# Performance work log

Measured on AMD Instinct MI355X. Metric: run time of the kernel, lower is better.

Reference implementation:

```python
import jax, jax.numpy as jnp
import numpy as np

EPS = 1e-6
K = 20
NEG_SLOPE = 0.2

def knn_idx(x, k):
    # x: (B, D, N) flattened vector features; returns (B, N, k) neighbor indices
    inner = -2.0 * jnp.einsum('bdn,bdm->bnm', x, x)
    xx = jnp.sum(x * x, axis=1)  # (B, N)
    pd = -xx[:, :, None] - inner - xx[:, None, :]  # negative squared distance
    _, idx = jax.lax.top_k(pd, k)
    return idx

def get_graph_feature(x, k):
    # x: (B, C, 3, N) -> (B, 2C, 3, N, k) edge features (nbr - ctr, ctr)
    B, C, _, N = x.shape
    idx = knn_idx(x.reshape(B, C * 3, N), k)           # (B, N, k)
    feat = jnp.transpose(x, (0, 3, 1, 2))              # (B, N, C, 3)
    nb = jax.vmap(lambda f, i: f[i])(feat, idx)        # (B, N, k, C, 3)
    ctr = jnp.broadcast_to(feat[:, :, None], nb.shape)
    out = jnp.concatenate([nb - ctr, ctr], axis=3)     # (B, N, k, 2C, 3)
    return jnp.transpose(out, (0, 3, 4, 1, 2))

def vn_batchnorm(x, gamma, beta):
    # x: (B, C, 3, ...); BatchNorm (training stats) applied to vector norms
    norm = jnp.linalg.norm(x, axis=2) + EPS            # (B, C, ...)
    axes = (0,) + tuple(range(2, norm.ndim))
    mu = jnp.mean(norm, axis=axes, keepdims=True)
    var = jnp.var(norm, axis=axes, keepdims=True)
    shape = (1, -1) + (1,) * (norm.ndim - 2)
    nbn = (norm - mu) / jnp.sqrt(var + 1e-5) * gamma.reshape(shape) + beta.reshape(shape)
    return x / norm[:, :, None] * nbn[:, :, None]

def vn_linear_leakyrelu(x, w_feat, w_dir, gamma, beta):
    # x: (B, Cin, 3, ...) -> (B, Cout, 3, ...)
    p = jnp.einsum('oc,bc...->bo...', w_feat, x)
    p = vn_batchnorm(p, gamma, beta)
    d = jnp.einsum('oc,bc...->bo...', w_dir, x)
    dot = jnp.sum(p * d, axis=2, keepdims=True)
    dsq = jnp.sum(d * d, axis=2, keepdims=True)
    proj = p - (dot / (dsq + EPS)) * d
    return NEG_SLOPE * p + (1.0 - NEG_SLOPE) * jnp.where(dot >= 0, p, proj)

def _forward(x, w1, d1, g1, b1, w2, d2, g2, b2, w3, d3, g3, b3, w4, d4, g4, b4, w5, d5, g5, b5):
    h = jnp.transpose(x, (0, 2, 1))[:, None]           # (B, 1, 3, N)
    h = vn_linear_leakyrelu(get_graph_feature(h, K), w1, d1, g1, b1)
    x1 = jnp.mean(h, axis=-1)                          # mean_pool over k: (B, 21, 3, N)
    h = vn_linear_leakyrelu(get_graph_feature(x1, K), w2, d2, g2, b2)
    x2 = jnp.mean(h, axis=-1)                          # (B, 21, 3, N)
    h = vn_linear_leakyrelu(get_graph_feature(x2, K), w3, d3, g3, b3)
    x3 = jnp.mean(h, axis=-1)                          # (B, 42, 3, N)
    h = vn_linear_leakyrelu(get_graph_feature(x3, K), w4, d4, g4, b4)
    x4 = jnp.mean(h, axis=-1)                          # (B, 85, 3, N)
    cat = jnp.concatenate([x1, x2, x3, x4], axis=1)    # (B, 169, 3, N)
    return vn_linear_leakyrelu(cat, w5, d5, g5, b5)    # (B, 341, 3, N)

def setup_inputs():
    key = jax.random.key(0)
    B, N = 8, 1024
    d = {"x": jax.random.normal(key, (B, N, 3), dtype=jnp.float32)}
    feat_shapes = {"1": (21, 2), "2": (21, 42), "3": (42, 42), "4": (85, 84), "5": (341, 169)}
    dir_out = {"1": 21, "2": 21, "3": 42, "4": 85, "5": 1}  # conv5 shares nonlinearity -> 1 dir channel
    for i, (name, (co, ci)) in enumerate(feat_shapes.items()):
        k1, k2 = jax.random.split(jax.random.fold_in(key, i + 1))
        s = 1.0 / np.sqrt(ci)
        d["w" + name] = jax.random.uniform(k1, (co, ci), minval=-s, maxval=s, dtype=jnp.float32)
        d["d" + name] = jax.random.uniform(k2, (dir_out[name], ci), minval=-s, maxval=s, dtype=jnp.float32)
        d["g" + name] = jnp.ones((co,), dtype=jnp.float32)
        d["b" + name] = jnp.zeros((co,), dtype=jnp.float32)
    return d

def reference(x, w1, d1, g1, b1, w2, d2, g2, b2, w3, d3, g3, b3, w4, d4, g4, b4, w5, d5, g5, b5):
    return _forward(x, w1, d1, g1, b1, w2, d2, g2, b2, w3, d3, g3, b3, w4, d4, g4, b4, w5, d5, g5, b5)
```

## Files before the change

### kernel.cpp

```cpp
#include <hip/hip_runtime.h>
#include <math.h>

#define KNN 20
#define NS 0.2f
#define EPSV 1e-6f
#define QT 4
#define OT 8
#define CROW 507
#define SSPLIT 8

extern __shared__ __align__(16) float smem[];

__global__ void k_transpose(const float* __restrict__ x, float* __restrict__ xt,
                            int B, int N) {
    int i = blockIdx.x * blockDim.x + threadIdx.x;
    if (i >= B * N) return;
    int b = i / N, n = i % N;
    const float* src = x + (size_t)(b * N + n) * 3;
    float* dst = xt + (size_t)b * 3 * N + n;
    dst[0] = src[0];
    dst[(size_t)N] = src[1];
    dst[(size_t)2 * N] = src[2];
}

__global__ void k_knn(const float* __restrict__ X, int* __restrict__ idx,
                      int N, int D, long batchStride, long sliceOff) {
    int b = blockIdx.y;
    int q0 = blockIdx.x * QT;
    int tid = threadIdx.x;
    int lane = tid & 63;
    int wave = tid >> 6;

    __shared__ __align__(16) float qf[128 * QT];
    __shared__ __align__(16) float pd[QT][1024];

    const float* Xb = X + (size_t)b * batchStride + sliceOff;

    for (int t = tid; t < QT * D; t += 256) {
        int d = t >> 2, q = t & 3;
        qf[d * QT + q] = Xb[(size_t)d * N + (q0 + q)];
    }
    __syncthreads();

    float a0x = 0.f, a0y = 0.f, a0z = 0.f, a0w = 0.f;
    float a1x = 0.f, a1y = 0.f, a1z = 0.f, a1w = 0.f;
    float a2x = 0.f, a2y = 0.f, a2z = 0.f, a2w = 0.f;
    float a3x = 0.f, a3y = 0.f, a3z = 0.f, a3w = 0.f;
    float m2x = 0.f, m2y = 0.f, m2z = 0.f, m2w = 0.f;
    float qn0 = 0.f, qn1 = 0.f, qn2 = 0.f, qn3 = 0.f;

    const float* mbase = Xb + 4 * tid;
#pragma unroll 3
    for (int d = 0; d < D; ++d) {
        float4 xm = *(const float4*)(mbase + (size_t)d * N);
        float4 qv = *(const float4*)(qf + d * QT);
        a0x += qv.x * xm.x; a0y += qv.x * xm.y; a0z += qv.x * xm.z; a0w += qv.x * xm.w;
        a1x += qv.y * xm.x; a1y += qv.y * xm.y; a1z += qv.y * xm.z; a1w += qv.y * xm.w;
        a2x += qv.z * xm.x; a2y += qv.z * xm.y; a2z += qv.z * xm.z; a2w += qv.z * xm.w;
        a3x += qv.w * xm.x; a3y += qv.w * xm.y; a3z += qv.w * xm.z; a3w += qv.w * xm.w;
        m2x += xm.x * xm.x; m2y += xm.y * xm.y; m2z += xm.z * xm.z; m2w += xm.w * xm.w;
        qn0 += qv.x * qv.x; qn1 += qv.y * qv.y; qn2 += qv.z * qv.z; qn3 += qv.w * qv.w;
    }

    {
        float4 v;
        v.x = 2.f * a0x - qn0 - m2x; v.y = 2.f * a0y - qn0 - m2y;
        v.z = 2.f * a0z - qn0 - m2z; v.w = 2.f * a0w - qn0 - m2w;
        *(float4*)&pd[0][4 * tid] = v;
        v.x = 2.f * a1x - qn1 - m2x; v.y = 2.f * a1y - qn1 - m2y;
        v.z = 2.f * a1z - qn1 - m2z; v.w = 2.f * a1w - qn1 - m2w;
        *(float4*)&pd[1][4 * tid] = v;
        v.x = 2.f * a2x - qn2 - m2x; v.y = 2.f * a2y - qn2 - m2y;
        v.z = 2.f * a2z - qn2 - m2z; v.w = 2.f * a2w - qn2 - m2w;
        *(float4*)&pd[2][4 * tid] = v;
        v.x = 2.f * a3x - qn3 - m2x; v.y = 2.f * a3y - qn3 - m2y;
        v.z = 2.f * a3z - qn3 - m2z; v.w = 2.f * a3w - qn3 - m2w;
        *(float4*)&pd[3][4 * tid] = v;
    }
    __syncthreads();

    float v[16];
#pragma unroll
    for (int t = 0; t < 16; ++t) v[t] = pd[wave][t * 64 + lane];

    long outBase = ((long)b * N + q0 + wave) * KNN;
    for (int it = 0; it < KNN; ++it) {
        float bv = v[0];
        int bi = lane;
#pragma unroll
        for (int t = 1; t < 16; ++t) {
            if (v[t] > bv) { bv = v[t]; bi = t * 64 + lane; }
        }
#pragma unroll
        for (int off = 32; off >= 1; off >>= 1) {
            float ov = __shfl_xor(bv, off, 64);
            int oi = __shfl_xor(bi, off, 64);
            if (ov > bv || (ov == bv && oi < bi)) { bv = ov; bi = oi; }
        }
        if (lane == 0) idx[outBase + it] = bi;
#pragma unroll
        for (int t = 0; t < 16; ++t) {
            if (bi == t * 64 + lane) v[t] = -INFINITY;
        }
    }
}

__global__ void k_matmul_pair_lds(const float* __restrict__ X, const float* __restrict__ W,
                                  const float* __restrict__ Dw,
                                  float* __restrict__ U, float* __restrict__ V,
                                  float* __restrict__ UD, float* __restrict__ VD,
                                  int C, int Co, int CoP, int TILE,
                                  int rowStride, int colOff) {
    const int CP = C * CoP;
    float* wts = smem;
    float* xs = smem + 4 * CP;

    int tid = threadIdx.x;
    int bn0 = blockIdx.x * TILE;
    int C3 = C * 3;

    int npad = CoP - Co;
    if (npad) {
        for (int t = tid; t < 4 * C * npad; t += 256) {
            int q = t / npad, oo = Co + t % npad;
            int mat = q / C, c = q % C;
            wts[mat * CP + c * CoP + oo] = 0.f;
        }
    }
    int twoCC = 2 * C * Co;
    for (int t = tid; t < twoCC; t += 256) {
        int o = t / (2 * C), c = t % (2 * C);
        float w = W[t], dw = Dw[t];
        if (c < C) {
            wts[c * CoP + o] = w;
            wts[2 * CP + c * CoP + o] = dw;
        } else {
            wts[CP + (c - C) * CoP + o] = w;
            wts[3 * CP + (c - C) * CoP + o] = dw;
        }
    }
    for (int t = tid; t < TILE * C3; t += 256) {
        int p = t / C3, cc = t % C3;
        xs[t] = X[(size_t)(bn0 + p) * rowStride + colOff + cc];
    }
    __syncthreads();
    for (int t = tid; t < CP; t += 256) {
        wts[CP + t] -= wts[t];
        wts[3 * CP + t] -= wts[2 * CP + t];
    }
    __syncthreads();

    int GPP = CoP >> 2;
    int items = TILE * GPP;
    for (int e = tid; e < items; e += 256) {
        int p = e / GPP, og = e - p * GPP;
        int o0 = og * 4;
        const float* xr = xs + p * C3;

        float aU[4][3], aV[4][3], aDu[4][3], aDv[4][3];
#pragma unroll
        for (int i = 0; i < 4; ++i)
#pragma unroll
            for (int j = 0; j < 3; ++j) {
                aU[i][j] = 0.f; aV[i][j] = 0.f; aDu[i][j] = 0.f; aDv[i][j] = 0.f;
            }

        for (int c = 0; c < C; ++c) {
            float x0 = xr[c * 3], x1 = xr[c * 3 + 1], x2 = xr[c * 3 + 2];
            const float* wp = wts + c * CoP + o0;
            float4 wa4 = *(const float4*)(wp);
            float4 wb4 = *(const float4*)(wp + CP);
            float4 da4 = *(const float4*)(wp + 2 * CP);
            float4 db4 = *(const float4*)(wp + 3 * CP);
            float wav[4] = {wa4.x, wa4.y, wa4.z, wa4.w};
            float wbv[4] = {wb4.x, wb4.y, wb4.z, wb4.w};
            float dav[4] = {da4.x, da4.y, da4.z, da4.w};
            float dbv[4] = {db4.x, db4.y, db4.z, db4.w};
#pragma unroll
            for (int i = 0; i < 4; ++i) {
                aU[i][0] += wav[i] * x0; aU[i][1] += wav[i] * x1; aU[i][2] += wav[i] * x2;
                aV[i][0] += wbv[i] * x0; aV[i][1] += wbv[i] * x1; aV[i][2] += wbv[i] * x2;
                aDu[i][0] += dav[i] * x0; aDu[i][1] += dav[i] * x1; aDu[i][2] += dav[i] * x2;
                aDv[i][0] += dbv[i] * x0; aDv[i][1] += dbv[i] * x1; aDv[i][2] += dbv[i] * x2;
            }
        }

        size_t base = ((size_t)(bn0 + p) * Co + o0) * 3;
#pragma unroll
        for (int i = 0; i < 4; ++i) {
            int o = o0 + i;
            if (o < Co) {
                size_t off = base + (size_t)i * 3;
                U[off] = aU[i][0]; U[off + 1] = aU[i][1]; U[off + 2] = aU[i][2];
                V[off] = aV[i][0]; V[off + 1] = aV[i][1]; V[off + 2] = aV[i][2];
                UD[off] = aDu[i][0]; UD[off + 1] = aDu[i][1]; UD[off + 2] = aDu[i][2];
                VD[off] = aDv[i][0]; VD[off + 1] = aDv[i][1]; VD[off + 2] = aDv[i][2];
            }
        }
    }
}

__global__ void k_stats_edge_det(const float* __restrict__ U, const float* __restrict__ V,
                                 const int* __restrict__ idx, float* __restrict__ partials,
                                 int N, int Co, int BN) {
    int o = blockIdx.x;
    int s = blockIdx.y;
    int tid = threadIdx.x;
    int P = BN / SSPLIT;
    int g0 = s * P;

    __shared__ float Ush[3072];
    __shared__ float r1[256], r2[256];

    for (int t = tid; t < P; t += 256) {
        const float* Ur = U + ((size_t)(g0 + t) * Co + o) * 3;
        Ush[t * 3 + 0] = Ur[0];
        Ush[t * 3 + 1] = Ur[1];
        Ush[t * 3 + 2] = Ur[2];
    }
    __syncthreads();

    float s1 = 0.f, s2 = 0.f;
    for (int pl = tid; pl < P; pl += 256) {
        int g = g0 + pl;
        const float* Vr = V + ((size_t)g * Co + o) * 3;
        float v0 = Vr[0], v1 = Vr[1], v2 = Vr[2];
        const int* ip = idx + (size_t)g * KNN;
        for (int kk = 0; kk < KNN; ++kk) {
            const float* Ur = Ush + ip[kk] * 3;
            float p0 = Ur[0] + v0;
            float p1 = Ur[1] + v1;
            float p2 = Ur[2] + v2;
            float nm = sqrtf(p0 * p0 + p1 * p1 + p2 * p2) + EPSV;
            s1 += nm;
            s2 += nm * nm;
        }
    }
    r1[tid] = s1; r2[tid] = s2;
    __syncthreads();
    for (int st = 128; st > 0; st >>= 1) {
        if (tid < st) { r1[tid] += r1[tid + st]; r2[tid] += r2[tid + st]; }
        __syncthreads();
    }
    if (tid == 0) {
        partials[(o * SSPLIT + s) * 2] = r1[0];
        partials[(o * SSPLIT + s) * 2 + 1] = r2[0];
    }
}

__global__ void k_final_edge_p(const float* __restrict__ U, const float* __restrict__ V,
                               const float* __restrict__ UD, const float* __restrict__ VD,
                               const int* __restrict__ idx, const float* __restrict__ partials,
                               const float* __restrict__ gamma, const float* __restrict__ beta,
                               float* __restrict__ catp,
                               int N, int Co, int colOff, float cnt, int total) {
    int g = blockIdx.x * 256 + threadIdx.x;
    if (g >= total) return;
    int o = g % Co;
    int r = g / Co;
    int n = r % N;
    int b = r / N;

    float s1 = 0.f, s2 = 0.f;
    for (int s = 0; s < SSPLIT; ++s) {
        s1 += partials[(o * SSPLIT + s) * 2];
        s2 += partials[(o * SSPLIT + s) * 2 + 1];
    }
    float mu = s1 / cnt;
    float var = s2 / cnt - mu * mu;
    float inv = rsqrtf(var + 1e-5f);
    float gmm = gamma[o], bt = beta[o];

    size_t ctr = ((size_t)(b * N + n) * Co + o) * 3;
    float v0 = V[ctr], v1 = V[ctr + 1], v2 = V[ctr + 2];
    float w0 = VD[ctr], w1 = VD[ctr + 1], w2 = VD[ctr + 2];
    const int* ip = idx + ((size_t)b * N + n) * KNN;

    float a0 = 0.f, a1 = 0.f, a2 = 0.f;
    for (int kk = 0; kk < KNN; ++kk) {
        int m = ip[kk];
        size_t nb = ((size_t)(b * N + m) * Co + o) * 3;
        float p0 = U[nb] + v0;
        float p1 = U[nb + 1] + v1;
        float p2 = U[nb + 2] + v2;
        float nm = sqrtf(p0 * p0 + p1 * p1 + p2 * p2) + EPSV;
        float nbn = (nm - mu) * inv * gmm + bt;
        float sc = nbn / nm;
        p0 *= sc; p1 *= sc; p2 *= sc;
        float d0 = UD[nb] + w0;
        float d1 = UD[nb + 1] + w1;
        float d2 = UD[nb + 2] + w2;
        float dot = p0 * d0 + p1 * d1 + p2 * d2;
        if (dot >= 0.f) {
            a0 += p0; a1 += p1; a2 += p2;
        } else {
            float f = dot / (d0 * d0 + d1 * d1 + d2 * d2 + EPSV);
            a0 += NS * p0 + (1.f - NS) * (p0 - f * d0);
            a1 += NS * p1 + (1.f - NS) * (p1 - f * d1);
            a2 += NS * p2 + (1.f - NS) * (p2 - f * d2);
        }
    }
    const float invk = 1.f / (float)KNN;
    float* outp = catp + (size_t)(b * N + n) * CROW + colOff + o * 3;
    outp[0] = a0 * invk;
    outp[1] = a1 * invk;
    outp[2] = a2 * invk;
}

__global__ void k_transpose_cat(const float* __restrict__ catp, float* __restrict__ catn,
                                int N, int c0, int CC) {
    __shared__ float tile[32][33];
    int b = blockIdx.z;
    int n0 = blockIdx.x * 32;
    int cb = blockIdx.y * 32;
    int tid = threadIdx.x;
    int tx = tid & 31, ty = tid >> 5;

#pragma unroll
    for (int rr = 0; rr < 4; ++rr) {
        int nl = ty + rr * 8;
        int c = cb + tx;
        if (c < CC)
            tile[nl][tx] = catp[(size_t)(b * N + n0 + nl) * CROW + c0 + c];
    }
    __syncthreads();
#pragma unroll
    for (int rr = 0; rr < 4; ++rr) {
        int cl = ty + rr * 8;
        int c = cb + cl;
        if (c < CC)
            catn[(size_t)b * CROW * N + (size_t)(c0 + c) * N + n0 + tx] = tile[tx][cl];
    }
}

__global__ void k_matmul_plain(const float* __restrict__ X, const float* __restrict__ W,
                               float* __restrict__ U,
                               int N, int Cin, int Cout, long batchStride, long sliceOff) {
    int j = blockIdx.y % 3;
    int ot = blockIdx.y / 3;
    int b = blockIdx.z;
    int o0 = ot * OT;
    int tid = threadIdx.x;
    int n = blockIdx.x * 256 + tid;

    __shared__ float wsm[OT][176];
    for (int t = tid; t < OT * Cin; t += 256) {
        int oo = t / Cin, c = t % Cin;
        int o = o0 + oo;
        wsm[oo][c] = (o < Cout) ? W[(size_t)o * Cin + c] : 0.f;
    }
    __syncthreads();

    const float* Xp = X + (size_t)b * batchStride + sliceOff + (size_t)j * N + n;
    float au[OT];
#pragma unroll
    for (int oo = 0; oo < OT; ++oo) au[oo] = 0.f;

    for (int c = 0; c < Cin; ++c) {
        float xv = Xp[(size_t)c * 3 * N];
#pragma unroll
        for (int oo = 0; oo < OT; ++oo) au[oo] += wsm[oo][c] * xv;
    }
#pragma unroll
    for (int oo = 0; oo < OT; ++oo) {
        int o = o0 + oo;
        if (o < Cout) U[(((size_t)b * Cout + o) * 3 + j) * N + n] = au[oo];
    }
}

__global__ void k_stats_plain_det(const float* __restrict__ U, float* __restrict__ mv,
                                  int N, int Cout, int BN, float cnt) {
    int o = blockIdx.x;
    int tid = threadIdx.x;
    float s1 = 0.f, s2 = 0.f;
    for (int g = tid; g < BN; g += 256) {
        int b = g / N, n = g % N;
        const float* Ub = U + (((size_t)b * Cout + o) * 3) * N;
        float p0 = Ub[n], p1 = Ub[(size_t)N + n], p2 = Ub[(size_t)2 * N + n];
        float nm = sqrtf(p0 * p0 + p1 * p1 + p2 * p2) + EPSV;
        s1 += nm;
        s2 += nm * nm;
    }
    __shared__ float r1[256], r2[256];
    r1[tid] = s1; r2[tid] = s2;
    __syncthreads();
    for (int st = 128; st > 0; st >>= 1) {
        if (tid < st) { r1[tid] += r1[tid + st]; r2[tid] += r2[tid + st]; }
        __syncthreads();
    }
    if (tid == 0) {
        float mu = r1[0] / cnt;
        float var = r2[0] / cnt - mu * mu;
        mv[2 * o] = mu;
        mv[2 * o + 1] = rsqrtf(var + 1e-5f);
    }
}

__global__ void k_final_plain(const float* __restrict__ U, const float* __restrict__ Dv,
                              const float* __restrict__ mv,
                              const float* __restrict__ gamma, const float* __restrict__ beta,
                              float* __restrict__ out, int N, int Cout) {
    int b = blockIdx.z, o = blockIdx.y, tid = threadIdx.x;
    int n = blockIdx.x * 256 + tid;
    float mu = mv[2 * o];
    float inv = mv[2 * o + 1];
    float g = gamma[o], bt = beta[o];

    const float* Ub = U + (((size_t)b * Cout + o) * 3) * N;
    float p0 = Ub[n], p1 = Ub[(size_t)N + n], p2 = Ub[(size_t)2 * N + n];
    float nm = sqrtf(p0 * p0 + p1 * p1 + p2 * p2) + EPSV;
    float nbn = (nm - mu) * inv * g + bt;
    float sc = nbn / nm;
    p0 *= sc; p1 *= sc; p2 *= sc;

    float d0 = Dv[((size_t)b * 3 + 0) * N + n];
    float d1 = Dv[((size_t)b * 3 + 1) * N + n];
    float d2 = Dv[((size_t)b * 3 + 2) * N + n];
    float dot = p0 * d0 + p1 * d1 + p2 * d2;
    float o0, o1, o2;
    if (dot >= 0.f) {
        o0 = p0; o1 = p1; o2 = p2;
    } else {
        float f = dot / (d0 * d0 + d1 * d1 + d2 * d2 + EPSV);
        o0 = NS * p0 + (1.f - NS) * (p0 - f * d0);
        o1 = NS * p1 + (1.f - NS) * (p1 - f * d1);
        o2 = NS * p2 + (1.f - NS) * (p2 - f * d2);
    }
    size_t ob = (((size_t)b * Cout + o) * 3) * N + n;
    out[ob] = o0;
    out[ob + (size_t)N] = o1;
    out[ob + (size_t)2 * N] = o2;
}

extern "C" void kernel_launch(void* const* d_in, const int* in_sizes, int n_in,
                              void* d_out, int out_size, void* d_ws, size_t ws_size,
                              hipStream_t stream) {
    (void)in_sizes; (void)n_in; (void)out_size; (void)ws_size;
    const int B = 8, N = 1024;

    const float* x = (const float*)d_in[0];
    const float* W[5]; const float* Dw[5]; const float* G[5]; const float* Bt[5];
    for (int l = 0; l < 5; ++l) {
        W[l]  = (const float*)d_in[1 + 4 * l];
        Dw[l] = (const float*)d_in[2 + 4 * l];
        G[l]  = (const float*)d_in[3 + 4 * l];
        Bt[l] = (const float*)d_in[4 + 4 * l];
    }

    float* ws = (float*)d_ws;
    size_t off = 0;
    float* xt = ws + off;     off += (size_t)B * 3 * N;
    int* idx = (int*)(ws + off); off += (size_t)B * N * KNN;
    float* catp = ws + off;   off += (size_t)B * N * CROW;
    float* catn = ws + off;   off += (size_t)B * N * CROW;
    float* Up = ws + off;     off += (size_t)B * N * 85 * 3;
    float* Vp = ws + off;     off += (size_t)B * N * 85 * 3;
    float* UDp = ws + off;    off += (size_t)B * N * 85 * 3;
    float* VDp = ws + off;    off += (size_t)B * N * 85 * 3;
    float* U5 = ws + off;     off += (size_t)B * 341 * 3 * N;
    float* d5buf = ws + off;  off += (size_t)B * 3 * N;
    float* partials = ws + off; off += (size_t)341 * SSPLIT * 2;
    float* mv = ws + off;     off += 2 * 341;

    k_transpose<<<(B * N + 255) / 256, 256, 0, stream>>>(x, xt, B, N);

    const int Cin_[4]  = {1, 21, 21, 42};
    const int Cout_[4] = {21, 21, 42, 85};
    const int inOff_[4] = {-1, 0, 21, 42};
    const int outOff_[4] = {0, 21, 42, 84};
    const int Tile_[4] = {32, 32, 32, 8};

    const int BN = B * N;

    for (int l = 0; l < 4; ++l) {
        int C = Cin_[l], Co = Cout_[l];
        int D = C * 3;
        int CoP = (Co + 3) & ~3;
        int TILE = Tile_[l];

        const float* Xn; long bs, so;
        if (inOff_[l] < 0) { Xn = xt; bs = (long)3 * N; so = 0; }
        else { Xn = catn; bs = (long)CROW * N; so = (long)inOff_[l] * 3 * N; }

        const float* Xp; int rs, co;
        if (inOff_[l] < 0) { Xp = x; rs = 3; co = 0; }
        else { Xp = catp; rs = CROW; co = inOff_[l] * 3; }

        dim3 gk(N / QT, B);
        k_knn<<<gk, 256, 0, stream>>>(Xn, idx, N, D, bs, so);

        size_t smemB = (size_t)(4 * C * CoP + TILE * C * 3) * sizeof(float);
        k_matmul_pair_lds<<<(B * N) / TILE, 256, smemB, stream>>>(
            Xp, W[l], Dw[l], Up, Vp, UDp, VDp, C, Co, CoP, TILE, rs, co);

        dim3 gst(Co, SSPLIT);
        k_stats_edge_det<<<gst, 256, 0, stream>>>(Up, Vp, idx, partials, N, Co, BN);

        int total = BN * Co;
        k_final_edge_p<<<(total + 255) / 256, 256, 0, stream>>>(
            Up, Vp, UDp, VDp, idx, partials, G[l], Bt[l], catp,
            N, Co, outOff_[l] * 3, (float)((size_t)BN * KNN), total);

        int CC = Co * 3;
        dim3 gt(N / 32, (CC + 31) / 32, B);
        k_transpose_cat<<<gt, 256, 0, stream>>>(catp, catn, N, outOff_[l] * 3, CC);
    }

    {
        long bs = (long)CROW * N, so = 0;
        dim3 gm5(N / 256, 3 * ((341 + OT - 1) / OT), B);
        k_matmul_plain<<<gm5, 256, 0, stream>>>(catn, W[4], U5, N, 169, 341, bs, so);
        dim3 gmd(N / 256, 3, B);
        k_matmul_plain<<<gmd, 256, 0, stream>>>(catn, Dw[4], d5buf, N, 169, 1, bs, so);
        k_stats_plain_det<<<341, 256, 0, stream>>>(U5, mv, N, 341, BN, (float)BN);
        dim3 gs5(N / 256, 341, B);
        k_final_plain<<<gs5, 256, 0, stream>>>(U5, d5buf, mv, G[4], Bt[4],
                                               (float*)d_out, N, 341);
    }
}
```

Before: 763.4 us.

## Precompute squared norms for kNN and rescan only the winning lane in top-k

Squared norms of all points are now computed once per layer, either in the transpose kernel or in a small new kernel. The kNN kernel reads them instead of recomputing query and candidate norms inside its distance loop, which removes redundant FMAs per block. The top-k selection keeps a per-lane running max and, after each of the 20 picks, only the lane that owned the winner masks it and rescans its 16 values. This replaces the full rescan in every lane. The cost is an extra kernel launch plus a global read of the norms per layer, and a divergent branch in the selection loop.

```diff
diff --git a/kernel.cpp b/kernel.cpp
--- a/kernel.cpp
+++ b/kernel.cpp
@@ -12,18 +12,38 @@
 extern __shared__ __align__(16) float smem[];
 
 __global__ void k_transpose(const float* __restrict__ x, float* __restrict__ xt,
-                            int B, int N) {
+                            float* __restrict__ xx, int B, int N) {
     int i = blockIdx.x * blockDim.x + threadIdx.x;
     if (i >= B * N) return;
     int b = i / N, n = i % N;
     const float* src = x + (size_t)(b * N + n) * 3;
     float* dst = xt + (size_t)b * 3 * N + n;
-    dst[0] = src[0];
-    dst[(size_t)N] = src[1];
-    dst[(size_t)2 * N] = src[2];
-}
-
-__global__ void k_knn(const float* __restrict__ X, int* __restrict__ idx,
+    float s0 = src[0], s1 = src[1], s2 = src[2];
+    dst[0] = s0;
+    dst[(size_t)N] = s1;
+    dst[(size_t)2 * N] = s2;
+    float s = 0.f;
+    s += s0 * s0;
+    s += s1 * s1;
+    s += s2 * s2;
+    xx[i] = s;
+}
+
+__global__ void k_sqnorm(const float* __restrict__ X, float* __restrict__ xx,
+                         int N, int D, long batchStride, long sliceOff) {
+    int i = blockIdx.x * 256 + threadIdx.x;
+    int b = i / N, n = i % N;
+    const float* Xb = X + (size_t)b * batchStride + sliceOff + n;
+    float s = 0.f;
+    for (int d = 0; d < D; ++d) {
+        float v = Xb[(size_t)d * N];
+        s += v * v;
+    }
+    xx[i] = s;
+}
+
+__global__ void k_knn(const float* __restrict__ X, const float* __restrict__ xx,
+                      int* __restrict__ idx,
                       int N, int D, long batchStride, long sliceOff) {
     int b = blockIdx.y;
     int q0 = blockIdx.x * QT;
@@ -35,6 +55,7 @@
     __shared__ __align__(16) float pd[QT][1024];
 
     const float* Xb = X + (size_t)b * batchStride + sliceOff;
+    const float* xxb = xx + (size_t)b * N;
 
     for (int t = tid; t < QT * D; t += 256) {
         int d = t >> 2, q = t & 3;
@@ -46,8 +67,6 @@
     float a1x = 0.f, a1y = 0.f, a1z = 0.f, a1w = 0.f;
     float a2x = 0.f, a2y = 0.f, a2z = 0.f, a2w = 0.f;
     float a3x = 0.f, a3y = 0.f, a3z = 0.f, a3w = 0.f;
-    float m2x = 0.f, m2y = 0.f, m2z = 0.f, m2w = 0.f;
-    float qn0 = 0.f, qn1 = 0.f, qn2 = 0.f, qn3 = 0.f;
 
     const float* mbase = Xb + 4 * tid;
 #pragma unroll 3
@@ -58,23 +77,23 @@
         a1x += qv.y * xm.x; a1y += qv.y * xm.y; a1z += qv.y * xm.z; a1w += qv.y * xm.w;
         a2x += qv.z * xm.x; a2y += qv.z * xm.y; a2z += qv.z * xm.z; a2w += qv.z * xm.w;
         a3x += qv.w * xm.x; a3y += qv.w * xm.y; a3z += qv.w * xm.z; a3w += qv.w * xm.w;
-        m2x += xm.x * xm.x; m2y += xm.y * xm.y; m2z += xm.z * xm.z; m2w += xm.w * xm.w;
-        qn0 += qv.x * qv.x; qn1 += qv.y * qv.y; qn2 += qv.z * qv.z; qn3 += qv.w * qv.w;
     }
 
     {
+        float4 m2 = *(const float4*)(xxb + 4 * tid);
+        float4 qn = *(const float4*)(xxb + q0);
         float4 v;
-        v.x = 2.f * a0x - qn0 - m2x; v.y = 2.f * a0y - qn0 - m2y;
-        v.z = 2.f * a0z - qn0 - m2z; v.w = 2.f * a0w - qn0 - m2w;
+        v.x = 2.f * a0x - qn.x - m2.x; v.y = 2.f * a0y - qn.x - m2.y;
+        v.z = 2.f * a0z - qn.x - m2.z; v.w = 2.f * a0w - qn.x - m2.w;
         *(float4*)&pd[0][4 * tid] = v;
-        v.x = 2.f * a1x - qn1 - m2x; v.y = 2.f * a1y - qn1 - m2y;
-        v.z = 2.f * a1z - qn1 - m2z; v.w = 2.f * a1w - qn1 - m2w;
+        v.x = 2.f * a1x - qn.y - m2.x; v.y = 2.f * a1y - qn.y - m2.y;
+        v.z = 2.f * a1z - qn.y - m2.z; v.w = 2.f * a1w - qn.y - m2.w;
         *(float4*)&pd[1][4 * tid] = v;
-        v.x = 2.f * a2x - qn2 - m2x; v.y = 2.f * a2y - qn2 - m2y;
-        v.z = 2.f * a2z - qn2 - m2z; v.w = 2.f * a2w - qn2 - m2w;
+        v.x = 2.f * a2x - qn.z - m2.x; v.y = 2.f * a2y - qn.z - m2.y;
+        v.z = 2.f * a2z - qn.z - m2.z; v.w = 2.f * a2w - qn.z - m2.w;
         *(float4*)&pd[2][4 * tid] = v;
-        v.x = 2.f * a3x - qn3 - m2x; v.y = 2.f * a3y - qn3 - m2y;
-        v.z = 2.f * a3z - qn3 - m2z; v.w = 2.f * a3w - qn3 - m2w;
+        v.x = 2.f * a3x - qn.w - m2.x; v.y = 2.f * a3y - qn.w - m2.y;
+        v.z = 2.f * a3z - qn.w - m2.z; v.w = 2.f * a3w - qn.w - m2.w;
         *(float4*)&pd[3][4 * tid] = v;
     }
     __syncthreads();
@@ -82,15 +101,18 @@
     float v[16];
 #pragma unroll
     for (int t = 0; t < 16; ++t) v[t] = pd[wave][t * 64 + lane];
+
+    float lv = v[0];
+    int li = lane;
+#pragma unroll
+    for (int t = 1; t < 16; ++t) {
+        if (v[t] > lv) { lv = v[t]; li = t * 64 + lane; }
+    }
 
     long outBase = ((long)b * N + q0 + wave) * KNN;
     for (int it = 0; it < KNN; ++it) {
-        float bv = v[0];
-        int bi = lane;
-#pragma unroll
-        for (int t = 1; t < 16; ++t) {
-            if (v[t] > bv) { bv = v[t]; bi = t * 64 + lane; }
-        }
+        float bv = lv;
+        int bi = li;
 #pragma unroll
         for (int off = 32; off >= 1; off >>= 1) {
             float ov = __shfl_xor(bv, off, 64);
@@ -98,9 +120,20 @@
             if (ov > bv || (ov == bv && oi < bi)) { bv = ov; bi = oi; }
         }
         if (lane == 0) idx[outBase + it] = bi;
-#pragma unroll
-        for (int t = 0; t < 16; ++t) {
-            if (bi == t * 64 + lane) v[t] = -INFINITY;
+
+        int sbi = __builtin_amdgcn_readfirstlane(bi);
+        if ((sbi & 63) == lane) {
+            int tt = sbi >> 6;
+#pragma unroll
+            for (int t = 0; t < 16; ++t) {
+                if (t == tt) v[t] = -INFINITY;
+            }
+            lv = v[0];
+            li = lane;
+#pragma unroll
+            for (int t = 1; t < 16; ++t) {
+                if (v[t] > lv) { lv = v[t]; li = t * 64 + lane; }
+            }
         }
     }
 }
@@ -459,10 +492,11 @@
     float* VDp = ws + off;    off += (size_t)B * N * 85 * 3;
     float* U5 = ws + off;     off += (size_t)B * 341 * 3 * N;
     float* d5buf = ws + off;  off += (size_t)B * 3 * N;
+    float* xx = ws + off;     off += (size_t)B * N;
     float* partials = ws + off; off += (size_t)341 * SSPLIT * 2;
     float* mv = ws + off;     off += 2 * 341;
 
-    k_transpose<<<(B * N + 255) / 256, 256, 0, stream>>>(x, xt, B, N);
+    k_transpose<<<(B * N + 255) / 256, 256, 0, stream>>>(x, xt, xx, B, N);
 
     const int Cin_[4]  = {1, 21, 21, 42};
     const int Cout_[4] = {21, 21, 42, 85};
@@ -486,8 +520,11 @@
         if (inOff_[l] < 0) { Xp = x; rs = 3; co = 0; }
         else { Xp = catp; rs = CROW; co = inOff_[l] * 3; }
 
+        if (inOff_[l] >= 0)
+            k_sqnorm<<<(B * N) / 256, 256, 0, stream>>>(Xn, xx, N, D, bs, so);
+
         dim3 gk(N / QT, B);
-        k_knn<<<gk, 256, 0, stream>>>(Xn, idx, N, D, bs, so);
+        k_knn<<<gk, 256, 0, stream>>>(Xn, xx, idx, N, D, bs, so);
 
         size_t smemB = (size_t)(4 * C * CoP + TILE * C * 3) * sizeof(float);
         k_matmul_pair_lds<<<(B * N) / TILE, 256, smemB, stream>>>(
```

After: 783.3 us. 2.6% more time.
